# Kernel optimization log

Measured on AMD Instinct MI355X. Metric: run time of the kernel, lower is better.

## Reference

```python
import jax, jax.numpy as jnp
import numpy as np

SEG = 2048      # segment_length
RATE = 4        # dilated_rate
DIM = 768
LN_EPS = 1e-5


def _sparsify(x):
    # b (l s) d -> b l s d, take every RATE-th within segment, flatten back
    b, L, d = x.shape
    x = x.reshape(b, L // SEG, SEG, d)[:, :, ::RATE]
    return x.reshape(b, -1, d)


def _layernorm(x, gamma, beta):
    mu = jnp.mean(x, axis=-1, keepdims=True)
    var = jnp.mean(jnp.square(x - mu), axis=-1, keepdims=True)
    return (x - mu) / jnp.sqrt(var + LN_EPS) * gamma + beta


def setup_inputs() -> dict:
    key = jax.random.key(0)
    ks = jax.random.split(key, 6)
    B, L, D = 4, 8192, DIM
    return {
        "Q": jax.random.normal(ks[0], (B, L, D), dtype=jnp.float32),
        "K": jax.random.normal(ks[1], (B, L, D), dtype=jnp.float32),
        "V": jax.random.normal(ks[2], (B, L, D), dtype=jnp.float32),
        "Wq": jax.random.normal(ks[3], (D, D), dtype=jnp.float32) * (1.0 / np.sqrt(D)),
        "Wk": jax.random.normal(ks[4], (D, D), dtype=jnp.float32) * (1.0 / np.sqrt(D)),
        "Wv": jax.random.normal(ks[5], (D, D), dtype=jnp.float32) * (1.0 / np.sqrt(D)),
        "ln_gamma": jnp.ones((D,), dtype=jnp.float32),
        "ln_beta": jnp.zeros((D,), dtype=jnp.float32),
    }


def reference(Q, K, V, Wq, Wk, Wv, ln_gamma, ln_beta):
    # strided segment dilation gather
    q = _sparsify(Q)  # [B, Ls, D], Ls = L/SEG * ceil(SEG/RATE)
    k = _sparsify(K)
    v = _sparsify(V)
    # linear projections (torch Linear: y = x @ W.T, no bias)
    q = q @ Wq.T
    k = k @ Wk.T
    v = v @ Wv.T
    # qk LayerNorm (shared norm module)
    q = _layernorm(q, ln_gamma, ln_beta)
    k = _layernorm(k, ln_gamma, ln_beta)
    # scaled dot product attention (non-causal, default scale 1/sqrt(D))
    scale = 1.0 / np.sqrt(q.shape[-1]).astype(np.float32)
    attn = jax.nn.softmax(jnp.einsum('bqd,bkd->bqk', q, k) * scale, axis=-1)
    out = jnp.einsum('bqk,bkd->bqd', attn, v)
    # dropout is identity in eval mode; final softmax over feature dim (as in source)
    return jax.nn.softmax(out, axis=-1)
```

## Files before the change

kernel.cpp:

```cpp
#include <hip/hip_runtime.h>
#include <math.h>

#define SEGLEN 2048
#define SRATE 4
#define DIM 768
#define BATCH 4
#define LFULL 8192
#define LSP 2048
#define NROWS (BATCH * LSP)
#define LN_EPS 1e-5f
#define ATT_SCALE 0.03608439182435161f

typedef __attribute__((ext_vector_type(8))) short s16x8;
typedef __attribute__((ext_vector_type(4))) float f32x4;

__device__ __forceinline__ ushort f2bf(float f) {
    unsigned u = __float_as_uint(f);
    u += 0x7fffu + ((u >> 16) & 1u);
    return (ushort)(u >> 16);
}
__device__ __forceinline__ float bf2f(ushort h) {
    return __uint_as_float(((unsigned)h) << 16);
}

__device__ __forceinline__ void ld_lds16(const ushort* g, ushort* l) {
    __builtin_amdgcn_global_load_lds(
        (const __attribute__((address_space(1))) void*)g,
        (__attribute__((address_space(3))) void*)l, 16, 0, 0);
}

__global__ void pack3(const float* __restrict__ Q, const float* __restrict__ Ks,
                      const float* __restrict__ V, ushort* __restrict__ X) {
    const float* src = blockIdx.z == 0 ? Q : blockIdx.z == 1 ? Ks : V;
    ushort* dst = X + (long)blockIdx.z * (NROWS * DIM);
    int idx = blockIdx.x * 256 + threadIdx.x;
    int r  = idx / (DIM / 4);
    int dg = idx - r * (DIM / 4);
    int bb = r >> 11;
    int s  = r & 2047;
    int seg = s >> 9;
    int j   = s & 511;
    long srow = (long)bb * LFULL + seg * SEGLEN + j * SRATE;
    float4 f = *(const float4*)(src + srow * DIM + dg * 4);
    ushort4 o;
    o.x = f2bf(f.x); o.y = f2bf(f.y); o.z = f2bf(f.z); o.w = f2bf(f.w);
    *(ushort4*)(dst + (long)r * DIM + dg * 4) = o;
}

__global__ void conv3(const float* __restrict__ Wq, const float* __restrict__ Wk,
                      const float* __restrict__ Wv, ushort* __restrict__ W) {
    const float* src = blockIdx.z == 0 ? Wq : blockIdx.z == 1 ? Wk : Wv;
    ushort* dst = W + (long)blockIdx.z * (DIM * DIM);
    int idx = blockIdx.x * 256 + threadIdx.x;
    float4 f = *(const float4*)(src + (long)idx * 4);
    ushort4 o;
    o.x = f2bf(f.x); o.y = f2bf(f.y); o.z = f2bf(f.z); o.w = f2bf(f.w);
    *(ushort4*)(dst + (long)idx * 4) = o;
}

template<int MODE, int NT>
__global__ __launch_bounds__(256, 2) void gemm_bt(
    const ushort* __restrict__ Ag, const ushort* __restrict__ Bg,
    ushort* __restrict__ Cb, ushort* __restrict__ Cb2,
    float* __restrict__ Cf, float* __restrict__ Cf2, float* __restrict__ lsum,
    int M, int N, int lda, int ldb, long sA, long sB, long sC,
    int ldc, float scale)
{
    __shared__ ushort lds[2][2][8192];
    const int K = NT * 64;

    const int gx = gridDim.x, gy = gridDim.y;
    const int G = gx * gy * gridDim.z;
    const int f = blockIdx.x + gx * (blockIdx.y + gy * blockIdx.z);
    const int wg = (f & 7) * (G >> 3) + (f >> 3);
    const int bx = wg % gx;
    const int rest = wg / gx;
    const int by = rest % gy;
    const int z  = rest / gy;

    const int bz = (MODE == 3) ? (z >> 1) : z;
    const int hz = (MODE == 3) ? (z & 1) : 0;
    const ushort* Aop = Ag + (long)bz * sA + (long)hz * K;
    const ushort* Bop = Bg + (long)bz * sB + (long)hz * K;

    const int tid = threadIdx.x;
    const int wid = tid >> 6, lane = tid & 63;
    const int wm = wid >> 1, wn = wid & 1;
    const int quad = lane >> 4, lr = lane & 15;
    const int rowBase = by * 128;
    const int colBase = bx * 128;

    int ib = ((lane & 15) << 6) | ((lane >> 4) << 4);
    ib ^= ((ib >> 9) & 1) << 5;

    long offA[4], offB[4];
#pragma unroll
    for (int i = 0; i < 4; i++) {
        int c = i * 256 + tid;
        int cc = c ^ (((c >> 5) & 1) << 1);
        int s = cc >> 6;
        int ks = s >> 3, gg = s & 7;
        int row  = gg * 16 + ((cc >> 2) & 15);
        int colE = ks * 32 + ((cc & 3) << 3);
        offA[i] = (long)(rowBase + row) * lda + colE;
        offB[i] = (long)(colBase + row) * ldb + colE;
    }

#define STA(buf, vv, i) ld_lds16(Aop + offA[i] + (long)(vv) * 64, &lds[buf][0][(i) * 2048 + wid * 512])
#define STB(buf, vv, i) ld_lds16(Bop + offB[i] + (long)(vv) * 64, &lds[buf][1][(i) * 2048 + wid * 512])

    STA(0, 0, 0); STA(0, 0, 1); STB(0, 0, 0); STB(0, 0, 1);
    STA(0, 0, 2); STA(0, 0, 3); STB(0, 0, 2); STB(0, 0, 3);
    STA(1, 1, 0); STA(1, 1, 1); STB(1, 1, 0); STB(1, 1, 1);

    f32x4 acc[4][4] = {};

    for (int v = 0; v < NT; ++v) {
        const int b = v & 1;
        const char* lA = (const char*)&lds[b][0][0];
        const char* lB = (const char*)&lds[b][1][0];

        if (v < NT - 1) asm volatile("s_waitcnt vmcnt(8)" ::: "memory");
        else            asm volatile("s_waitcnt vmcnt(4)" ::: "memory");
        __builtin_amdgcn_s_barrier();
        if (v + 1 < NT) {
            STA(b ^ 1, v + 1, 2); STA(b ^ 1, v + 1, 3);
            STB(b ^ 1, v + 1, 2); STB(b ^ 1, v + 1, 3);
        }
        {
            s16x8 af[4], bfm[4];
#pragma unroll
            for (int t = 0; t < 4; ++t)
                af[t] = *(const s16x8*)(lA + ((0 * 8 + wm * 4 + t) << 10) + ib);
#pragma unroll
            for (int t = 0; t < 4; ++t)
                bfm[t] = *(const s16x8*)(lB + ((0 * 8 + wn * 4 + t) << 10) + ib);
            __builtin_amdgcn_s_setprio(1);
#pragma unroll
            for (int i = 0; i < 4; i++)
#pragma unroll
                for (int j = 0; j < 4; j++)
                    acc[i][j] = __builtin_amdgcn_mfma_f32_16x16x32_bf16(
                        af[i], bfm[j], acc[i][j], 0, 0, 0);
            __builtin_amdgcn_s_setprio(0);
        }

        if (v < NT - 1) asm volatile("s_waitcnt vmcnt(8)" ::: "memory");
        else            asm volatile("s_waitcnt vmcnt(0)" ::: "memory");
        __builtin_amdgcn_s_barrier();
        if (v + 2 < NT) {
            STA(b, v + 2, 0); STA(b, v + 2, 1);
            STB(b, v + 2, 0); STB(b, v + 2, 1);
        }
        {
            s16x8 af[4], bfm[4];
#pragma unroll
            for (int t = 0; t < 4; ++t)
                af[t] = *(const s16x8*)(lA + ((1 * 8 + wm * 4 + t) << 10) + ib);
#pragma unroll
            for (int t = 0; t < 4; ++t)
                bfm[t] = *(const s16x8*)(lB + ((1 * 8 + wn * 4 + t) << 10) + ib);
            __builtin_amdgcn_s_setprio(1);
#pragma unroll
            for (int i = 0; i < 4; i++)
#pragma unroll
                for (int j = 0; j < 4; j++)
                    acc[i][j] = __builtin_amdgcn_mfma_f32_16x16x32_bf16(
                        af[i], bfm[j], acc[i][j], 0, 0, 0);
            __builtin_amdgcn_s_setprio(0);
        }
    }
#undef STA
#undef STB

    if (MODE == 0) {
        if (z < 2) {
            ushort* Cz = Cb + (long)z * sC;
#pragma unroll
            for (int i = 0; i < 4; i++) {
                int r0 = rowBase + wm * 64 + i * 16 + quad * 4;
#pragma unroll
                for (int j = 0; j < 4; j++) {
                    int c = colBase + wn * 64 + j * 16 + lr;
#pragma unroll
                    for (int reg = 0; reg < 4; reg++)
                        Cz[(long)(r0 + reg) * ldc + c] = f2bf(acc[i][j][reg]);
                }
            }
        } else {
#pragma unroll
            for (int i = 0; i < 4; i++) {
                int r0 = rowBase + wm * 64 + i * 16 + quad * 4;
                int bidx = r0 >> 11;
                int jj = r0 & 2047;
                ushort* Cz = Cb2 + (long)bidx * DIM * LSP;
#pragma unroll
                for (int j = 0; j < 4; j++) {
                    int c = colBase + wn * 64 + j * 16 + lr;
                    ushort4 o;
                    o.x = f2bf(acc[i][j][0]); o.y = f2bf(acc[i][j][1]);
                    o.z = f2bf(acc[i][j][2]); o.w = f2bf(acc[i][j][3]);
                    *(ushort4*)(Cz + (long)c * LSP + jj) = o;
                }
            }
        }
    } else if (MODE == 2) {
        ushort* Cz = Cb + (long)z * sC;
        float* lz = lsum + (long)z * M;
#pragma unroll
        for (int i = 0; i < 4; i++) {
            int r0 = rowBase + wm * 64 + i * 16 + quad * 4;
#pragma unroll
            for (int reg = 0; reg < 4; reg++) {
                float s = 0.f;
#pragma unroll
                for (int j = 0; j < 4; j++) {
                    int c = colBase + wn * 64 + j * 16 + lr;
                    float e = __expf(acc[i][j][reg] * scale);
                    s += e;
                    Cz[(long)(r0 + reg) * ldc + c] = f2bf(e);
                }
                for (int m = 1; m < 16; m <<= 1) s += __shfl_xor(s, m, 64);
                if (lr == 0) atomicAdd(&lz[r0 + reg], s);
            }
        }
    } else {
        float* Cz = (hz ? Cf2 : Cf) + (long)bz * sC;
#pragma unroll
        for (int i = 0; i < 4; i++) {
            int r0 = rowBase + wm * 64 + i * 16 + quad * 4;
#pragma unroll
            for (int j = 0; j < 4; j++) {
                int c = colBase + wn * 64 + j * 16 + lr;
#pragma unroll
                for (int reg = 0; reg < 4; reg++)
                    Cz[(long)(r0 + reg) * ldc + c] = acc[i][j][reg];
            }
        }
    }
}

__global__ __launch_bounds__(256) void ln_inplace(
    ushort* __restrict__ X, const float* __restrict__ gamma,
    const float* __restrict__ beta)
{
    int wid = threadIdx.x >> 6, lane = threadIdx.x & 63;
    int row = blockIdx.x * 4 + wid;
    ushort* xp = X + (long)row * DIM;
    float v[12];
    float s = 0.f;
#pragma unroll
    for (int c = 0; c < 12; c++) { v[c] = bf2f(xp[c * 64 + lane]); s += v[c]; }
    for (int m = 1; m < 64; m <<= 1) s += __shfl_xor(s, m, 64);
    float mean = s * (1.0f / 768.0f);
    float q = 0.f;
#pragma unroll
    for (int c = 0; c < 12; c++) { float d = v[c] - mean; q += d * d; }
    for (int m = 1; m < 64; m <<= 1) q += __shfl_xor(q, m, 64);
    float rstd = rsqrtf(q * (1.0f / 768.0f) + LN_EPS);
#pragma unroll
    for (int c = 0; c < 12; c++) {
        int idx = c * 64 + lane;
        float y = (v[c] - mean) * rstd * gamma[idx] + beta[idx];
        xp[idx] = f2bf(y);
    }
}

__global__ __launch_bounds__(256) void final_softmax(
    const float* __restrict__ O0, const float* __restrict__ O1,
    const float* __restrict__ l, float* __restrict__ out)
{
    int wid = threadIdx.x >> 6, lane = threadIdx.x & 63;
    int row = blockIdx.x * 4 + wid;
    long base = (long)row * DIM;
    float inv = 1.0f / l[row];
    float v[12]; float mx = -1e30f;
#pragma unroll
    for (int c = 0; c < 12; c++) {
        v[c] = (O0[base + c * 64 + lane] + O1[base + c * 64 + lane]) * inv;
        mx = fmaxf(mx, v[c]);
    }
    for (int m = 1; m < 64; m <<= 1) mx = fmaxf(mx, __shfl_xor(mx, m, 64));
    float s = 0.f;
#pragma unroll
    for (int c = 0; c < 12; c++) { v[c] = __expf(v[c] - mx); s += v[c]; }
    for (int m = 1; m < 64; m <<= 1) s += __shfl_xor(s, m, 64);
    float invs = 1.0f / s;
#pragma unroll
    for (int c = 0; c < 12; c++) out[base + c * 64 + lane] = v[c] * invs;
}

extern "C" void kernel_launch(void* const* d_in, const int* in_sizes, int n_in,
                              void* d_out, int out_size, void* d_ws, size_t ws_size,
                              hipStream_t stream)
{
    const float* Q  = (const float*)d_in[0];
    const float* K_ = (const float*)d_in[1];
    const float* V  = (const float*)d_in[2];
    const float* Wq = (const float*)d_in[3];
    const float* Wk = (const float*)d_in[4];
    const float* Wv = (const float*)d_in[5];
    const float* g  = (const float*)d_in[6];
    const float* b  = (const float*)d_in[7];
    float* out = (float*)d_out;

    char* ws = (char*)d_ws;
    ushort* Xq  = (ushort*)(ws + 0);
    ushort* Wqb = (ushort*)(ws + 37748736);
    ushort* qb  = (ushort*)(ws + 41287680);
    ushort* kb  = (ushort*)(ws + 53870592);
    ushort* vT  = (ushort*)(ws + 66453504);
    float*  O0  = (float*)(ws + 79036416);
    float*  l   = (float*)(ws + 104202240);
    ushort* P   = (ushort*)(ws + 0);
    float*  O1  = (float*)(ws + 41287680);

    (void)in_sizes; (void)n_in; (void)out_size; (void)ws_size;

    hipMemsetAsync(l, 0, NROWS * sizeof(float), stream);

    pack3<<<dim3(6144, 1, 3), 256, 0, stream>>>(Q, K_, V, Xq);
    conv3<<<dim3(576, 1, 3), 256, 0, stream>>>(Wq, Wk, Wv, Wqb);

    gemm_bt<0, 12><<<dim3(DIM / 128, NROWS / 128, 3), 256, 0, stream>>>(
        Xq, Wqb, qb, vT, nullptr, nullptr, nullptr,
        NROWS, DIM, DIM, DIM,
        (long)NROWS * DIM, (long)DIM * DIM, (long)NROWS * DIM, DIM, 0.f);

    ln_inplace<<<4096, 256, 0, stream>>>(qb, g, b);

    gemm_bt<2, 12><<<dim3(LSP / 128, LSP / 128, BATCH), 256, 0, stream>>>(
        qb, kb, P, nullptr, nullptr, nullptr, l,
        LSP, LSP, DIM, DIM,
        (long)LSP * DIM, (long)LSP * DIM, (long)LSP * LSP, LSP, ATT_SCALE);

    gemm_bt<3, 16><<<dim3(DIM / 128, LSP / 128, BATCH * 2), 256, 0, stream>>>(
        P, vT, nullptr, nullptr, O0, O1, nullptr,
        LSP, DIM, LSP, LSP,
        (long)LSP * LSP, (long)DIM * LSP, (long)LSP * DIM, DIM, 0.f);

    final_softmax<<<2048, 256, 0, stream>>>(O0, O1, l, out);
}
```

Before: 383.8 us.

## Use 512-thread GEMM blocks, fuse weight conversion into pack, vectorize LN/softmax

The GEMM now runs 8 waves per 128x128 tile instead of 4. Each wave computes a 32x64 sub-tile with half the accumulators, and each thread issues fewer global-to-LDS loads per stage. The weight bf16 conversion is merged into the activation pack kernel as a fourth z-slice, which removes one launch. LayerNorm and the final softmax switch to contiguous per-lane vector loads and stores. Together these aim to raise latency hiding and occupancy and cut launch and memory-instruction overhead, at the cost of more barrier participants and less register-level reuse per wave.

```diff
diff --git a/kernel.cpp b/kernel.cpp
--- a/kernel.cpp
+++ b/kernel.cpp
@@ -29,11 +29,26 @@
         (__attribute__((address_space(3))) void*)l, 16, 0, 0);
 }
 
-__global__ void pack3(const float* __restrict__ Q, const float* __restrict__ Ks,
-                      const float* __restrict__ V, ushort* __restrict__ X) {
-    const float* src = blockIdx.z == 0 ? Q : blockIdx.z == 1 ? Ks : V;
-    ushort* dst = X + (long)blockIdx.z * (NROWS * DIM);
+__global__ void pack4(const float* __restrict__ Q, const float* __restrict__ Ks,
+                      const float* __restrict__ V, const float* __restrict__ Wq,
+                      const float* __restrict__ Wk, const float* __restrict__ Wv,
+                      ushort* __restrict__ X, ushort* __restrict__ W) {
+    const int z = blockIdx.z;
     int idx = blockIdx.x * 256 + threadIdx.x;
+    if (z == 3) {
+        if (idx < 3 * (DIM * DIM / 4)) {
+            int ww = idx / (DIM * DIM / 4);
+            int r = idx - ww * (DIM * DIM / 4);
+            const float* src = ww == 0 ? Wq : ww == 1 ? Wk : Wv;
+            float4 f = *(const float4*)(src + (long)r * 4);
+            ushort4 o;
+            o.x = f2bf(f.x); o.y = f2bf(f.y); o.z = f2bf(f.z); o.w = f2bf(f.w);
+            *(ushort4*)(W + (long)ww * DIM * DIM + (long)r * 4) = o;
+        }
+        return;
+    }
+    const float* src = z == 0 ? Q : z == 1 ? Ks : V;
+    ushort* dst = X + (long)z * (NROWS * DIM);
     int r  = idx / (DIM / 4);
     int dg = idx - r * (DIM / 4);
     int bb = r >> 11;
@@ -47,19 +62,8 @@
     *(ushort4*)(dst + (long)r * DIM + dg * 4) = o;
 }
 
-__global__ void conv3(const float* __restrict__ Wq, const float* __restrict__ Wk,
-                      const float* __restrict__ Wv, ushort* __restrict__ W) {
-    const float* src = blockIdx.z == 0 ? Wq : blockIdx.z == 1 ? Wk : Wv;
-    ushort* dst = W + (long)blockIdx.z * (DIM * DIM);
-    int idx = blockIdx.x * 256 + threadIdx.x;
-    float4 f = *(const float4*)(src + (long)idx * 4);
-    ushort4 o;
-    o.x = f2bf(f.x); o.y = f2bf(f.y); o.z = f2bf(f.z); o.w = f2bf(f.w);
-    *(ushort4*)(dst + (long)idx * 4) = o;
-}
-
 template<int MODE, int NT>
-__global__ __launch_bounds__(256, 2) void gemm_bt(
+__global__ __launch_bounds__(512, 4) void gemm_bt(
     const ushort* __restrict__ Ag, const ushort* __restrict__ Bg,
     ushort* __restrict__ Cb, ushort* __restrict__ Cb2,
     float* __restrict__ Cf, float* __restrict__ Cf2, float* __restrict__ lsum,
@@ -84,8 +88,8 @@
     const ushort* Bop = Bg + (long)bz * sB + (long)hz * K;
 
     const int tid = threadIdx.x;
-    const int wid = tid >> 6, lane = tid & 63;
-    const int wm = wid >> 1, wn = wid & 1;
+    const int w = tid >> 6, lane = tid & 63;
+    const int wm = w >> 1, wn = w & 1;
     const int quad = lane >> 4, lr = lane & 15;
     const int rowBase = by * 128;
     const int colBase = bx * 128;
@@ -93,80 +97,72 @@
     int ib = ((lane & 15) << 6) | ((lane >> 4) << 4);
     ib ^= ((ib >> 9) & 1) << 5;
 
-    long offA[4], offB[4];
-#pragma unroll
-    for (int i = 0; i < 4; i++) {
-        int c = i * 256 + tid;
+    long offA, offB;
+    {
+        int c = tid;
         int cc = c ^ (((c >> 5) & 1) << 1);
         int s = cc >> 6;
-        int ks = s >> 3, gg = s & 7;
-        int row  = gg * 16 + ((cc >> 2) & 15);
-        int colE = ks * 32 + ((cc & 3) << 3);
-        offA[i] = (long)(rowBase + row) * lda + colE;
-        offB[i] = (long)(colBase + row) * ldb + colE;
+        int row  = s * 16 + ((cc >> 2) & 15);
+        int colE = (cc & 3) << 3;
+        offA = (long)(rowBase + row) * lda + colE;
+        offB = (long)(colBase + row) * ldb + colE;
     }
 
-#define STA(buf, vv, i) ld_lds16(Aop + offA[i] + (long)(vv) * 64, &lds[buf][0][(i) * 2048 + wid * 512])
-#define STB(buf, vv, i) ld_lds16(Bop + offB[i] + (long)(vv) * 64, &lds[buf][1][(i) * 2048 + wid * 512])
-
-    STA(0, 0, 0); STA(0, 0, 1); STB(0, 0, 0); STB(0, 0, 1);
-    STA(0, 0, 2); STA(0, 0, 3); STB(0, 0, 2); STB(0, 0, 3);
-    STA(1, 1, 0); STA(1, 1, 1); STB(1, 1, 0); STB(1, 1, 1);
-
-    f32x4 acc[4][4] = {};
+#define STA(buf, vv, h) ld_lds16(Aop + offA + (long)(vv) * 64 + (h) * 32, &lds[buf][0][(h) * 4096 + w * 512])
+#define STB(buf, vv, h) ld_lds16(Bop + offB + (long)(vv) * 64 + (h) * 32, &lds[buf][1][(h) * 4096 + w * 512])
+
+    STA(0, 0, 0); STB(0, 0, 0);
+    STA(0, 0, 1); STB(0, 0, 1);
+    STA(1, 1, 0); STB(1, 1, 0);
+
+    f32x4 acc[2][4] = {};
 
     for (int v = 0; v < NT; ++v) {
         const int b = v & 1;
         const char* lA = (const char*)&lds[b][0][0];
         const char* lB = (const char*)&lds[b][1][0];
 
-        if (v < NT - 1) asm volatile("s_waitcnt vmcnt(8)" ::: "memory");
-        else            asm volatile("s_waitcnt vmcnt(4)" ::: "memory");
+        if (v < NT - 1) asm volatile("s_waitcnt vmcnt(4)" ::: "memory");
+        else            asm volatile("s_waitcnt vmcnt(2)" ::: "memory");
         __builtin_amdgcn_s_barrier();
-        if (v + 1 < NT) {
-            STA(b ^ 1, v + 1, 2); STA(b ^ 1, v + 1, 3);
-            STB(b ^ 1, v + 1, 2); STB(b ^ 1, v + 1, 3);
-        }
+        if (v + 1 < NT) { STA(b ^ 1, v + 1, 1); STB(b ^ 1, v + 1, 1); }
         {
-            s16x8 af[4], bfm[4];
-#pragma unroll
-            for (int t = 0; t < 4; ++t)
-                af[t] = *(const s16x8*)(lA + ((0 * 8 + wm * 4 + t) << 10) + ib);
-#pragma unroll
-            for (int t = 0; t < 4; ++t)
-                bfm[t] = *(const s16x8*)(lB + ((0 * 8 + wn * 4 + t) << 10) + ib);
+            s16x8 aq[2], bq[4];
+#pragma unroll
+            for (int i = 0; i < 2; ++i)
+                aq[i] = *(const s16x8*)(lA + ((wm * 2 + i) << 10) + ib);
+#pragma unroll
+            for (int j = 0; j < 4; ++j)
+                bq[j] = *(const s16x8*)(lB + ((wn * 4 + j) << 10) + ib);
             __builtin_amdgcn_s_setprio(1);
 #pragma unroll
-            for (int i = 0; i < 4; i++)
+            for (int i = 0; i < 2; i++)
 #pragma unroll
                 for (int j = 0; j < 4; j++)
                     acc[i][j] = __builtin_amdgcn_mfma_f32_16x16x32_bf16(
-                        af[i], bfm[j], acc[i][j], 0, 0, 0);
+                        aq[i], bq[j], acc[i][j], 0, 0, 0);
             __builtin_amdgcn_s_setprio(0);
         }
 
-        if (v < NT - 1) asm volatile("s_waitcnt vmcnt(8)" ::: "memory");
+        if (v < NT - 1) asm volatile("s_waitcnt vmcnt(4)" ::: "memory");
         else            asm volatile("s_waitcnt vmcnt(0)" ::: "memory");
         __builtin_amdgcn_s_barrier();
-        if (v + 2 < NT) {
-            STA(b, v + 2, 0); STA(b, v + 2, 1);
-            STB(b, v + 2, 0); STB(b, v + 2, 1);
-        }
+        if (v + 2 < NT) { STA(b, v + 2, 0); STB(b, v + 2, 0); }
         {
-            s16x8 af[4], bfm[4];
-#pragma unroll
-            for (int t = 0; t < 4; ++t)
-                af[t] = *(const s16x8*)(lA + ((1 * 8 + wm * 4 + t) << 10) + ib);
-#pragma unroll
-            for (int t = 0; t < 4; ++t)
-                bfm[t] = *(const s16x8*)(lB + ((1 * 8 + wn * 4 + t) << 10) + ib);
+            s16x8 aq[2], bq[4];
+#pragma unroll
+            for (int i = 0; i < 2; ++i)
+                aq[i] = *(const s16x8*)(lA + ((8 + wm * 2 + i) << 10) + ib);
+#pragma unroll
+            for (int j = 0; j < 4; ++j)
+                bq[j] = *(const s16x8*)(lB + ((8 + wn * 4 + j) << 10) + ib);
             __builtin_amdgcn_s_setprio(1);
 #pragma unroll
-            for (int i = 0; i < 4; i++)
+            for (int i = 0; i < 2; i++)
 #pragma unroll
                 for (int j = 0; j < 4; j++)
                     acc[i][j] = __builtin_amdgcn_mfma_f32_16x16x32_bf16(
-                        af[i], bfm[j], acc[i][j], 0, 0, 0);
+                        aq[i], bq[j], acc[i][j], 0, 0, 0);
             __builtin_amdgcn_s_setprio(0);
         }
     }
@@ -177,8 +173,8 @@
         if (z < 2) {
             ushort* Cz = Cb + (long)z * sC;
 #pragma unroll
-            for (int i = 0; i < 4; i++) {
-                int r0 = rowBase + wm * 64 + i * 16 + quad * 4;
+            for (int i = 0; i < 2; i++) {
+                int r0 = rowBase + wm * 32 + i * 16 + quad * 4;
 #pragma unroll
                 for (int j = 0; j < 4; j++) {
                     int c = colBase + wn * 64 + j * 16 + lr;
@@ -189,8 +185,8 @@
             }
         } else {
 #pragma unroll
-            for (int i = 0; i < 4; i++) {
-                int r0 = rowBase + wm * 64 + i * 16 + quad * 4;
+            for (int i = 0; i < 2; i++) {
+                int r0 = rowBase + wm * 32 + i * 16 + quad * 4;
                 int bidx = r0 >> 11;
                 int jj = r0 & 2047;
                 ushort* Cz = Cb2 + (long)bidx * DIM * LSP;
@@ -208,8 +204,8 @@
         ushort* Cz = Cb + (long)z * sC;
         float* lz = lsum + (long)z * M;
 #pragma unroll
-        for (int i = 0; i < 4; i++) {
-            int r0 = rowBase + wm * 64 + i * 16 + quad * 4;
+        for (int i = 0; i < 2; i++) {
+            int r0 = rowBase + wm * 32 + i * 16 + quad * 4;
 #pragma unroll
             for (int reg = 0; reg < 4; reg++) {
                 float s = 0.f;
@@ -227,8 +223,8 @@
     } else {
         float* Cz = (hz ? Cf2 : Cf) + (long)bz * sC;
 #pragma unroll
-        for (int i = 0; i < 4; i++) {
-            int r0 = rowBase + wm * 64 + i * 16 + quad * 4;
+        for (int i = 0; i < 2; i++) {
+            int r0 = rowBase + wm * 32 + i * 16 + quad * 4;
 #pragma unroll
             for (int j = 0; j < 4; j++) {
                 int c = colBase + wn * 64 + j * 16 + lr;
@@ -246,11 +242,17 @@
 {
     int wid = threadIdx.x >> 6, lane = threadIdx.x & 63;
     int row = blockIdx.x * 4 + wid;
-    ushort* xp = X + (long)row * DIM;
+    ushort* xp = X + (long)row * DIM + lane * 12;
+    ushort4 a0 = *(const ushort4*)xp;
+    ushort4 a1 = *(const ushort4*)(xp + 4);
+    ushort4 a2 = *(const ushort4*)(xp + 8);
     float v[12];
+    v[0] = bf2f(a0.x); v[1] = bf2f(a0.y); v[2]  = bf2f(a0.z); v[3]  = bf2f(a0.w);
+    v[4] = bf2f(a1.x); v[5] = bf2f(a1.y); v[6]  = bf2f(a1.z); v[7]  = bf2f(a1.w);
+    v[8] = bf2f(a2.x); v[9] = bf2f(a2.y); v[10] = bf2f(a2.z); v[11] = bf2f(a2.w);
     float s = 0.f;
 #pragma unroll
-    for (int c = 0; c < 12; c++) { v[c] = bf2f(xp[c * 64 + lane]); s += v[c]; }
+    for (int c = 0; c < 12; c++) s += v[c];
     for (int m = 1; m < 64; m <<= 1) s += __shfl_xor(s, m, 64);
     float mean = s * (1.0f / 768.0f);
     float q = 0.f;
@@ -258,12 +260,18 @@
     for (int c = 0; c < 12; c++) { float d = v[c] - mean; q += d * d; }
     for (int m = 1; m < 64; m <<= 1) q += __shfl_xor(q, m, 64);
     float rstd = rsqrtf(q * (1.0f / 768.0f) + LN_EPS);
-#pragma unroll
-    for (int c = 0; c < 12; c++) {
-        int idx = c * 64 + lane;
-        float y = (v[c] - mean) * rstd * gamma[idx] + beta[idx];
-        xp[idx] = f2bf(y);
-    }
+    const float* gp = gamma + lane * 12;
+    const float* bp = beta + lane * 12;
+    float4 g0 = *(const float4*)gp, g1 = *(const float4*)(gp + 4), g2 = *(const float4*)(gp + 8);
+    float4 b0 = *(const float4*)bp, b1 = *(const float4*)(bp + 4), b2 = *(const float4*)(bp + 8);
+    float gg[12] = {g0.x,g0.y,g0.z,g0.w,g1.x,g1.y,g1.z,g1.w,g2.x,g2.y,g2.z,g2.w};
+    float bb[12] = {b0.x,b0.y,b0.z,b0.w,b1.x,b1.y,b1.z,b1.w,b2.x,b2.y,b2.z,b2.w};
+    ushort o[12];
+#pragma unroll
+    for (int c = 0; c < 12; c++)
+        o[c] = f2bf((v[c] - mean) * rstd * gg[c] + bb[c]);
+    ushort4 w0 = {o[0],o[1],o[2],o[3]}, w1 = {o[4],o[5],o[6],o[7]}, w2 = {o[8],o[9],o[10],o[11]};
+    *(ushort4*)xp = w0; *(ushort4*)(xp + 4) = w1; *(ushort4*)(xp + 8) = w2;
 }
 
 __global__ __launch_bounds__(256) void final_softmax(
@@ -272,22 +280,31 @@
 {
     int wid = threadIdx.x >> 6, lane = threadIdx.x & 63;
     int row = blockIdx.x * 4 + wid;
-    long base = (long)row * DIM;
+    long base = (long)row * DIM + lane * 12;
     float inv = 1.0f / l[row];
-    float v[12]; float mx = -1e30f;
-#pragma unroll
-    for (int c = 0; c < 12; c++) {
-        v[c] = (O0[base + c * 64 + lane] + O1[base + c * 64 + lane]) * inv;
-        mx = fmaxf(mx, v[c]);
-    }
+    float4 p0 = *(const float4*)(O0 + base);
+    float4 p1 = *(const float4*)(O0 + base + 4);
+    float4 p2 = *(const float4*)(O0 + base + 8);
+    float4 q0 = *(const float4*)(O1 + base);
+    float4 q1 = *(const float4*)(O1 + base + 4);
+    float4 q2 = *(const float4*)(O1 + base + 8);
+    float v[12] = {p0.x+q0.x, p0.y+q0.y, p0.z+q0.z, p0.w+q0.w,
+                   p1.x+q1.x, p1.y+q1.y, p1.z+q1.z, p1.w+q1.w,
+                   p2.x+q2.x, p2.y+q2.y, p2.z+q2.z, p2.w+q2.w};
+    float mx = -1e30f;
+#pragma unroll
+    for (int c = 0; c < 12; c++) { v[c] *= inv; mx = fmaxf(mx, v[c]); }
     for (int m = 1; m < 64; m <<= 1) mx = fmaxf(mx, __shfl_xor(mx, m, 64));
     float s = 0.f;
 #pragma unroll
     for (int c = 0; c < 12; c++) { v[c] = __expf(v[c] - mx); s += v[c]; }
     for (int m = 1; m < 64; m <<= 1) s += __shfl_xor(s, m, 64);
     float invs = 1.0f / s;
-#pragma unroll
-    for (int c = 0; c < 12; c++) out[base + c * 64 + lane] = v[c] * invs;
+    float4 w0 = {v[0]*invs, v[1]*invs, v[2]*invs, v[3]*invs};
+    float4 w1 = {v[4]*invs, v[5]*invs, v[6]*invs, v[7]*invs};
+    float4 w2 = {v[8]*invs, v[9]*invs, v[10]*invs, v[11]*invs};
+    float* op = out + base;
+    *(float4*)op = w0; *(float4*)(op + 4) = w1; *(float4*)(op + 8) = w2;
 }
 
 extern "C" void kernel_launch(void* const* d_in, const int* in_sizes, int n_in,
@@ -319,22 +336,21 @@
 
     hipMemsetAsync(l, 0, NROWS * sizeof(float), stream);
 
-    pack3<<<dim3(6144, 1, 3), 256, 0, stream>>>(Q, K_, V, Xq);
-    conv3<<<dim3(576, 1, 3), 256, 0, stream>>>(Wq, Wk, Wv, Wqb);
-
-    gemm_bt<0, 12><<<dim3(DIM / 128, NROWS / 128, 3), 256, 0, stream>>>(
+    pack4<<<dim3(6144, 1, 4), 256, 0, stream>>>(Q, K_, V, Wq, Wk, Wv, Xq, Wqb);
+
+    gemm_bt<0, 12><<<dim3(DIM / 128, NROWS / 128, 3), 512, 0, stream>>>(
         Xq, Wqb, qb, vT, nullptr, nullptr, nullptr,
         NROWS, DIM, DIM, DIM,
         (long)NROWS * DIM, (long)DIM * DIM, (long)NROWS * DIM, DIM, 0.f);
 
     ln_inplace<<<4096, 256, 0, stream>>>(qb, g, b);
 
-    gemm_bt<2, 12><<<dim3(LSP / 128, LSP / 128, BATCH), 256, 0, stream>>>(
+    gemm_bt<2, 12><<<dim3(LSP / 128, LSP / 128, BATCH), 512, 0, stream>>>(
         qb, kb, P, nullptr, nullptr, nullptr, l,
         LSP, LSP, DIM, DIM,
         (long)LSP * DIM, (long)LSP * DIM, (long)LSP * LSP, LSP, ATT_SCALE);
 
-    gemm_bt<3, 16><<<dim3(DIM / 128, LSP / 128, BATCH * 2), 256, 0, stream>>>(
+    gemm_bt<3, 16><<<dim3(DIM / 128, LSP / 128, BATCH * 2), 512, 0, stream>>>(
         P, vT, nullptr, nullptr, O0, O1, nullptr,
         LSP, DIM, LSP, LSP,
         (long)LSP * LSP, (long)DIM * LSP, (long)LSP * DIM, DIM, 0.f);
```

Measured after the change: 384.2 us. About the same (+0.1%).
